# Kernel tuning notes

Hardware: AMD Instinct MI355X
Metric: run time of the kernel (lower is better)

## Reference

```python
import jax, jax.numpy as jnp
import numpy as np

N = 32768      # nodes
E = 524288     # edges (avg degree 16)
F = 64         # node_feat_dim
D = 64         # gnn_dim (= per-head out channels, concat=False)
ED = 32        # edge_feat_dim
L = 6          # num_layers
H = 2          # heads
C = D          # per-head channels
LN_EPS = 1e-5


def layer_norm(h, g, b):
    mu = jnp.mean(h, axis=-1, keepdims=True)
    var = jnp.mean((h - mu) ** 2, axis=-1, keepdims=True)
    return g * (h - mu) * jax.lax.rsqrt(var + LN_EPS) + b


def setup_inputs() -> dict:
    key = jax.random.key(0)
    ks = jax.random.split(key, 16)
    x = jax.random.normal(ks[0], (N, F), jnp.float32)
    edge_index = jax.random.randint(ks[1], (2, E), 0, N, jnp.int32)
    edge_attr = jax.random.normal(ks[2], (E, ED), jnp.float32)
    manual_gamma = 1.0 + 0.1 * jax.random.normal(ks[3], (L, D), jnp.float32)
    manual_beta = 0.1 * jax.random.normal(ks[4], (L, D), jnp.float32)
    # node_embed Linear(F, D)
    embed_W = jax.random.normal(ks[5], (F, D), jnp.float32) / np.float32(np.sqrt(F))
    embed_b = jnp.zeros((D,), jnp.float32)
    # per-layer LayerNorm affine params
    ln_gamma = jnp.ones((L, D), jnp.float32)
    ln_beta = jnp.zeros((L, D), jnp.float32)
    # per-layer GATConv params (shared lin for src/dst, PyG non-bipartite)
    lin_W = jax.random.normal(ks[6], (L, D, H * C), jnp.float32) / np.float32(np.sqrt(D))
    lin_edge_W = jax.random.normal(ks[7], (L, ED, H * C), jnp.float32) / np.float32(np.sqrt(ED))
    att_src = jax.random.normal(ks[8], (L, H, C), jnp.float32) / np.float32(np.sqrt(C))
    att_dst = jax.random.normal(ks[9], (L, H, C), jnp.float32) / np.float32(np.sqrt(C))
    att_edge = jax.random.normal(ks[10], (L, H, C), jnp.float32) / np.float32(np.sqrt(C))
    gat_bias = jnp.zeros((L, C), jnp.float32)
    # edge output head: Linear(2D+ED, D) -> ReLU -> Linear(D, 1)
    head_W1 = jax.random.normal(ks[11], (2 * D + ED, D), jnp.float32) / np.float32(np.sqrt(2 * D + ED))
    head_b1 = jnp.zeros((D,), jnp.float32)
    head_W2 = jax.random.normal(ks[12], (D, 1), jnp.float32) / np.float32(np.sqrt(D))
    head_b2 = jnp.zeros((1,), jnp.float32)
    return dict(x=x, edge_index=edge_index, edge_attr=edge_attr,
                manual_gamma=manual_gamma, manual_beta=manual_beta,
                embed_W=embed_W, embed_b=embed_b, ln_gamma=ln_gamma, ln_beta=ln_beta,
                lin_W=lin_W, lin_edge_W=lin_edge_W, att_src=att_src, att_dst=att_dst,
                att_edge=att_edge, gat_bias=gat_bias, head_W1=head_W1, head_b1=head_b1,
                head_W2=head_W2, head_b2=head_b2)


def reference(x, edge_index, edge_attr, manual_gamma, manual_beta,
              embed_W, embed_b, ln_gamma, ln_beta, lin_W, lin_edge_W,
              att_src, att_dst, att_edge, gat_bias, head_W1, head_b1,
              head_W2, head_b2):
    src, dst = edge_index[0], edge_index[1]
    # PyG GATConv default add_self_loops=True, fill_value='mean' for edge_attr
    loop = jnp.arange(N, dtype=edge_index.dtype)
    src_f = jnp.concatenate([src, loop])   # [E+N]
    dst_f = jnp.concatenate([dst, loop])
    deg = jax.ops.segment_sum(jnp.ones((E,), x.dtype), dst, num_segments=N)
    loop_attr = jax.ops.segment_sum(edge_attr, dst, num_segments=N) / jnp.maximum(deg, 1.0)[:, None]
    edge_attr_f = jnp.concatenate([edge_attr, loop_attr], axis=0)  # [E+N, ED]

    h = x @ embed_W + embed_b  # [N, D]
    for l in range(L):
        hn = layer_norm(h, ln_gamma[l], ln_beta[l])
        hm = manual_gamma[l][None, :] * hn + manual_beta[l][None, :]
        xh = (hm @ lin_W[l]).reshape(N, H, C)                      # [N,H,C]
        a_s = jnp.sum(xh * att_src[l][None], axis=-1)              # [N,H]
        a_d = jnp.sum(xh * att_dst[l][None], axis=-1)              # [N,H]
        eh = (edge_attr_f @ lin_edge_W[l]).reshape(-1, H, C)       # [E+N,H,C]
        a_e = jnp.sum(eh * att_edge[l][None], axis=-1)             # [E+N,H]
        alpha = jax.nn.leaky_relu(a_s[src_f] + a_d[dst_f] + a_e, 0.2)
        amax = jax.ops.segment_max(alpha, dst_f, num_segments=N)   # every node has a self-loop
        ex = jnp.exp(alpha - amax[dst_f])
        den = jax.ops.segment_sum(ex, dst_f, num_segments=N)
        w = ex / (den[dst_f] + 1e-16)                              # segment softmax [E+N,H]
        msg = xh[src_f] * w[..., None]                             # [E+N,H,C]
        out = jax.ops.segment_sum(msg, dst_f, num_segments=N)      # [N,H,C]
        h = jax.nn.relu(jnp.mean(out, axis=1) + gat_bias[l])       # concat=False -> head mean

    ef = jnp.concatenate([h[src], h[dst], edge_attr], axis=-1)     # [E, 2D+ED]
    hid = jax.nn.relu(ef @ head_W1 + head_b1)
    return (hid @ head_W2 + head_b2)[:, 0]                         # [E]
```

## Files before the change

### kernel.cpp

```cpp
#include <hip/hip_runtime.h>
#include <hip/hip_bf16.h>
#include <math.h>

#define NN 32768
#define EE 524288
#define LL 6

typedef __attribute__((ext_vector_type(8))) short short8;
typedef __attribute__((ext_vector_type(4))) float floatx4;

union U16x8 { short8 v; unsigned short u[8]; };

__device__ __forceinline__ unsigned short f2bf(float x) {
    union { float f; unsigned int u; } v; v.f = x;
    unsigned int r = v.u + 0x7fffu + ((v.u >> 16) & 1u);
    return (unsigned short)(r >> 16);
}
__device__ __forceinline__ float bf2f(unsigned short h) {
    union { unsigned int u; float f; } v; v.u = (unsigned int)h << 16;
    return v.f;
}


__global__ void deg_kernel(const int* __restrict__ dst, int* __restrict__ deg) {
    int e = blockIdx.x * 256 + threadIdx.x;
    if (e < EE) atomicAdd(&deg[dst[e]], 1);
}

__global__ __launch_bounds__(1024) void scan_kernel(const int* __restrict__ deg,
                                                    int* __restrict__ row_ptr) {
    __shared__ int bs[1024];
    int t = threadIdx.x;
    int base = t * 32;
    int loc[32];
    int s = 0;
#pragma unroll
    for (int i = 0; i < 32; ++i) { int v = deg[base + i]; loc[i] = s; s += v; }
    bs[t] = s;
    __syncthreads();
    for (int off = 1; off < 1024; off <<= 1) {
        int v = (t >= off) ? bs[t - off] : 0;
        __syncthreads();
        bs[t] += v;
        __syncthreads();
    }
    int pre = (t == 0) ? 0 : bs[t - 1];
#pragma unroll
    for (int i = 0; i < 32; ++i) row_ptr[base + i] = pre + loc[i];
    if (t == 1023) row_ptr[NN] = bs[1023];
}

__global__ void fill_kernel(const int* __restrict__ src, const int* __restrict__ dst,
                            const int* __restrict__ row_ptr, int* __restrict__ cnt,
                            int2* __restrict__ sedge) {
    int e = blockIdx.x * 256 + threadIdx.x;
    if (e >= EE) return;
    int d = dst[e];
    int pos = row_ptr[d] + atomicAdd(&cnt[d], 1);
    sedge[pos] = make_int2(src[e], e);
}

__global__ void vmake_kernel(const float* __restrict__ lin_edge_W,
                             const float* __restrict__ att_edge,
                             float* __restrict__ v) {
    int t = threadIdx.x;
    if (t >= 384) return;
    int l = t >> 6; int r = t & 63; int ed = r >> 1; int hh = r & 1;
    const float* w = lin_edge_W + l * 32 * 128 + ed * 128 + hh * 64;
    const float* a = att_edge + l * 128 + hh * 64;
    float s = 0.f;
#pragma unroll 8
    for (int c = 0; c < 64; ++c) s += w[c] * a[c];
    v[t] = s;
}

__global__ void vsmake_kernel(const float* __restrict__ lin_W,
                              const float* __restrict__ att_src,
                              const float* __restrict__ att_dst,
                              float* __restrict__ vs, float* __restrict__ vvd) {
    int l = blockIdx.x;
    int tid = threadIdx.x;
    int sel = tid >> 7, idx = tid & 127;
    int h = idx >> 6, k = idx & 63;
    const float* att = (sel ? att_dst : att_src) + l * 128 + h * 64;
    const float* wr = lin_W + ((size_t)l * 64 + k) * 128 + h * 64;
    float s = 0.f;
#pragma unroll 8
    for (int c = 0; c < 64; ++c) s += wr[c] * att[c];
    (sel ? vvd : vs)[l * 128 + idx] = s;
}

__global__ void ae_kernel(const float* __restrict__ edge_attr,
                          const float* __restrict__ v,
                          float* __restrict__ aeo) {
    __shared__ float sv[384];
    int tid = threadIdx.x;
    for (int i = tid; i < 384; i += 128) sv[i] = v[i];
    __syncthreads();
    int e = blockIdx.x * 128 + tid;
    if (e >= EE) return;
    float ea[32];
    const float4* p = (const float4*)(edge_attr + (size_t)e * 32);
#pragma unroll
    for (int i = 0; i < 8; ++i) {
        float4 f = p[i];
        ea[4 * i] = f.x; ea[4 * i + 1] = f.y; ea[4 * i + 2] = f.z; ea[4 * i + 3] = f.w;
    }
#pragma unroll
    for (int l = 0; l < LL; ++l) {
        float s0 = 0.f, s1 = 0.f;
#pragma unroll
        for (int ed = 0; ed < 32; ++ed) {
            float x = ea[ed];
            s0 += x * sv[l * 64 + ed * 2];
            s1 += x * sv[l * 64 + ed * 2 + 1];
        }
        aeo[((size_t)l * EE + e) * 2] = s0;
        aeo[((size_t)l * EE + e) * 2 + 1] = s1;
    }
}

__global__ __launch_bounds__(256) void embed_ln_kernel(
    const float* __restrict__ x, const float* __restrict__ W, const float* __restrict__ b,
    const float* __restrict__ ln_g, const float* __restrict__ ln_b,
    const float* __restrict__ mg, const float* __restrict__ mb,
    const float* __restrict__ vs0, const float* __restrict__ vd0,
    unsigned short* __restrict__ hm_bf, float* __restrict__ a_s, float* __restrict__ a_d) {
    __shared__ float xr[4][64];
    int w = threadIdx.x >> 6, j = threadIdx.x & 63;
    int n = blockIdx.x * 4 + w;
    xr[w][j] = x[(size_t)n * 64 + j];
    __syncthreads();
    float acc = b[j];
#pragma unroll 8
    for (int k = 0; k < 64; ++k) acc += xr[w][k] * W[k * 64 + j];
    float s = acc, sq = acc * acc;
    for (int off = 1; off < 64; off <<= 1) { s += __shfl_xor(s, off); sq += __shfl_xor(sq, off); }
    float mu = s * (1.f / 64.f);
    float var = sq * (1.f / 64.f) - mu * mu;
    float rs = rsqrtf(var + 1e-5f);
    float hm = mg[j] * (ln_g[j] * (acc - mu) * rs + ln_b[j]) + mb[j];
    hm_bf[(size_t)n * 64 + j] = f2bf(hm);
    float s0 = hm * vs0[j], s1 = hm * vs0[64 + j];
    float d0 = hm * vd0[j], d1 = hm * vd0[64 + j];
    for (int off = 1; off < 64; off <<= 1) {
        s0 += __shfl_xor(s0, off); s1 += __shfl_xor(s1, off);
        d0 += __shfl_xor(d0, off); d1 += __shfl_xor(d1, off);
    }
    if (j == 0) {
        a_s[n * 2] = s0; a_s[n * 2 + 1] = s1;
        a_d[n * 2] = d0; a_d[n * 2 + 1] = d1;
    }
}

__global__ __launch_bounds__(256) void wprep_kernel(const float* __restrict__ lin_W,
                                                    const float* __restrict__ head_W1,
                                                    unsigned short* __restrict__ gBhi,
                                                    unsigned short* __restrict__ gBlo) {
    int bb = blockIdx.x;
    int tid = threadIdx.x;
    unsigned short* dh = gBhi + (size_t)bb * 128 * 64;
    unsigned short* dl = gBlo + (size_t)bb * 128 * 64;
    if (bb < 6) {
        int n2 = tid & 63, kh = tid >> 6;
        U16x8 hh[4], ll[4];
        for (int kk = 0; kk < 32; ++kk) {
            int j = kh * 32 + kk;
            int h = j >> 6, k = j & 63;
            float wv = 0.5f * lin_W[((size_t)bb * 64 + k) * 128 + h * 64 + n2];
            unsigned short h16 = f2bf(wv);
            hh[kk >> 3].u[kk & 7] = h16;
            ll[kk >> 3].u[kk & 7] = f2bf(wv - bf2f(h16));
        }
#pragma unroll
        for (int c = 0; c < 4; ++c) {
            int cg = kh * 4 + c;
            int off = n2 * 128 + ((cg ^ (n2 & 15)) << 3);
            *(short8*)(dh + off) = hh[c].v;
            *(short8*)(dl + off) = ll[c].v;
        }
    } else {
        int n = tid & 127, kh = tid >> 7;
        U16x8 hh[4], ll[4];
        for (int kk = 0; kk < 32; ++kk) {
            int k = kh * 32 + kk;
            float wv = (n < 64) ? head_W1[k * 64 + n] : head_W1[(64 + k) * 64 + (n - 64)];
            unsigned short h16 = f2bf(wv);
            hh[kk >> 3].u[kk & 7] = h16;
            ll[kk >> 3].u[kk & 7] = f2bf(wv - bf2f(h16));
        }
#pragma unroll
        for (int c = 0; c < 4; ++c) {
            int cg = kh * 4 + c;
            int off = n * 64 + ((cg ^ (n & 7)) << 3);
            *(short8*)(dh + off) = hh[c].v;
            *(short8*)(dl + off) = ll[c].v;
        }
    }
}

__device__ __forceinline__ void fma8(uint4 pv, float w0, float w1, float* a0, float* a1) {
    unsigned int u[4] = {pv.x, pv.y, pv.z, pv.w};
#pragma unroll
    for (int j = 0; j < 4; ++j) {
        union { unsigned int q; float f; } lo, hi;
        lo.q = u[j] << 16; hi.q = u[j] & 0xffff0000u;
        a0[2 * j] += w0 * lo.f;  a1[2 * j] += w1 * lo.f;
        a0[2 * j + 1] += w0 * hi.f;  a1[2 * j + 1] += w1 * hi.f;
    }
}

__global__ __launch_bounds__(256) void aggregate5_kernel(
    const unsigned short* __restrict__ hm_bf, const float* __restrict__ a_s,
    const float* __restrict__ a_d, const float* __restrict__ aeo,
    const int* __restrict__ row_ptr, const int2* __restrict__ sedge,
    unsigned short* __restrict__ Abf) {
    __shared__ float2 swg[4][64];
    __shared__ int ssv[4][64];
    int w = threadIdx.x >> 6, lane = threadIdx.x & 63;
    int n = blockIdx.x * 4 + w;
    int slot = lane >> 3, ch = lane & 7;
    const float2* as2 = (const float2*)a_s;
    const float2* ae2 = (const float2*)aeo;
    const uint4* hmv = (const uint4*)hm_bf;
    float2 adn = ((const float2*)a_d)[n];
    float2 asn = as2[n];
    uint4 pvself = hmv[(size_t)n * 8 + ch];
    int beg = row_ptr[n], end = row_ptr[n + 1];

    float acc0[8] = {}, acc1[8] = {};
    float den0 = 0.f, den1 = 0.f, aex = 0.f, aey = 0.f;

    for (int cs = beg; cs < end; cs += 64) {
        int cnt = min(64, end - cs);
        float2 wpair = make_float2(0.f, 0.f);
        int sval = n;
        if (lane < cnt) {
            int2 se = sedge[cs + lane];
            float2 ae = ae2[se.y];
            float2 as = as2[se.x];
            aex += ae.x; aey += ae.y;
            float al0 = as.x + adn.x + ae.x; al0 = al0 > 0.f ? al0 : 0.2f * al0;
            float al1 = as.y + adn.y + ae.y; al1 = al1 > 0.f ? al1 : 0.2f * al1;
            wpair = make_float2(__expf(al0), __expf(al1));
            sval = se.x;
        }
        swg[w][lane] = wpair;
        ssv[w][lane] = sval;
        int ng2 = (cnt + 15) >> 4;
        for (int g2 = 0; g2 < ng2; ++g2) {
            int eA = g2 * 16 + slot, eB = g2 * 16 + 8 + slot;
            float2 wA = swg[w][eA];
            float2 wB = swg[w][eB];
            int svA = ssv[w][eA];
            int svB = ssv[w][eB];
            uint4 pvA = hmv[(size_t)svA * 8 + ch];
            uint4 pvB = hmv[(size_t)svB * 8 + ch];
            fma8(pvA, wA.x, wA.y, acc0, acc1);
            den0 += wA.x; den1 += wA.y;
            fma8(pvB, wB.x, wB.y, acc0, acc1);
            den0 += wB.x; den1 += wB.y;
        }
    }
#pragma unroll
    for (int m = 8; m < 64; m <<= 1) {
#pragma unroll
        for (int j = 0; j < 8; ++j) {
            acc0[j] += __shfl_xor(acc0[j], m);
            acc1[j] += __shfl_xor(acc1[j], m);
        }
        den0 += __shfl_xor(den0, m);
        den1 += __shfl_xor(den1, m);
        aex += __shfl_xor(aex, m);
        aey += __shfl_xor(aey, m);
    }
    if (slot == 0) {
        float invd = 1.f / fmaxf((float)(end - beg), 1.f);
        float al0 = asn.x + adn.x + aex * invd; al0 = al0 > 0.f ? al0 : 0.2f * al0;
        float al1 = asn.y + adn.y + aey * invd; al1 = al1 > 0.f ? al1 : 0.2f * al1;
        float ws0 = __expf(al0), ws1 = __expf(al1);
        fma8(pvself, ws0, ws1, acc0, acc1);
        den0 += ws0; den1 += ws1;
        float inv0 = 1.f / (den0 + 1e-16f), inv1 = 1.f / (den1 + 1e-16f);
        U16x8 h0, h1;
#pragma unroll
        for (int j = 0; j < 8; ++j) {
            h0.u[j] = f2bf(acc0[j] * inv0);
            h1.u[j] = f2bf(acc1[j] * inv1);
        }
        int i15 = n & 15;
        unsigned short* row = Abf + (size_t)n * 128;
        *(short8*)(row + ((ch ^ i15) << 3)) = h0.v;
        *(short8*)(row + (((8 + ch) ^ i15) << 3)) = h1.v;
    }
}

template <int LAST>
__global__ __launch_bounds__(256) void post_gemm(
    const unsigned short* __restrict__ Abf, const unsigned short* __restrict__ gBhi,
    const unsigned short* __restrict__ gBlo, const float* __restrict__ bias,
    const float* __restrict__ ln_g, const float* __restrict__ ln_b,
    const float* __restrict__ mg, const float* __restrict__ mb,
    const float* __restrict__ vsn, const float* __restrict__ vdn,
    unsigned short* __restrict__ hm_bf, float* __restrict__ a_s, float* __restrict__ a_d,
    float* __restrict__ hbuf) {
    __shared__ unsigned short Ahi[64 * 128];
    __shared__ unsigned short Bhi[64 * 128], Blo[64 * 128];
    int tid = threadIdx.x;
    {
        const uint4* sa = (const uint4*)(Abf + (size_t)blockIdx.x * 64 * 128);
        const uint4* sh = (const uint4*)gBhi;
        const uint4* sl = (const uint4*)gBlo;
        for (int i = tid; i < 1024; i += 256) {
            ((uint4*)Ahi)[i] = sa[i];
            ((uint4*)Bhi)[i] = sh[i];
            ((uint4*)Blo)[i] = sl[i];
        }
    }
    __syncthreads();

    int w = tid >> 6, lane = tid & 63, col = lane & 15, quad = lane >> 4;
    int m = w * 16 + col;
    floatx4 acc[4] = {};
#pragma unroll
    for (int s = 0; s < 4; ++s) {
        int ca = (quad + 4 * s) ^ col;
        short8 ahi = *(const short8*)(Ahi + m * 128 + ca * 8);
#pragma unroll
        for (int t = 0; t < 4; ++t) {
            int off = (t * 16 + col) * 128 + ca * 8;
            short8 bhi = *(const short8*)(Bhi + off);
            short8 blo = *(const short8*)(Blo + off);
            acc[t] = __builtin_amdgcn_mfma_f32_16x16x32_bf16(ahi, blo, acc[t], 0, 0, 0);
            acc[t] = __builtin_amdgcn_mfma_f32_16x16x32_bf16(ahi, bhi, acc[t], 0, 0, 0);
        }
    }
    int nodebase = blockIdx.x * 64 + w * 16;
    float bv[4];
#pragma unroll
    for (int t = 0; t < 4; ++t) bv[t] = bias[t * 16 + col];
    if (LAST) {
#pragma unroll
        for (int t = 0; t < 4; ++t)
#pragma unroll
            for (int r = 0; r < 4; ++r) {
                float hv = acc[t][r] + bv[t];
                hv = hv > 0.f ? hv : 0.f;
                hbuf[(size_t)(nodebase + quad * 4 + r) * 64 + t * 16 + col] = hv;
            }
    } else {
        float vsv[4], vsv1[4], vdv[4], vdv1[4], lg[4], lb[4], mgv[4], mbv[4];
#pragma unroll
        for (int t = 0; t < 4; ++t) {
            int c = t * 16 + col;
            vsv[t] = vsn[c]; vsv1[t] = vsn[64 + c];
            vdv[t] = vdn[c]; vdv1[t] = vdn[64 + c];
            lg[t] = ln_g[c]; lb[t] = ln_b[c];
            mgv[t] = mg[c]; mbv[t] = mb[c];
        }
#pragma unroll
        for (int r = 0; r < 4; ++r) {
            int node = nodebase + quad * 4 + r;
            float hv[4];
            float s = 0.f, sq = 0.f;
#pragma unroll
            for (int t = 0; t < 4; ++t) {
                float v = acc[t][r] + bv[t];
                v = v > 0.f ? v : 0.f;
                hv[t] = v;
                s += v; sq += v * v;
            }
            for (int off = 1; off < 16; off <<= 1) { s += __shfl_xor(s, off); sq += __shfl_xor(sq, off); }
            float mu = s * (1.f / 64.f);
            float var = sq * (1.f / 64.f) - mu * mu;
            float rs = rsqrtf(var + 1e-5f);
            float s0 = 0.f, s1 = 0.f, d0 = 0.f, d1 = 0.f;
#pragma unroll
            for (int t = 0; t < 4; ++t) {
                float hmv = mgv[t] * (lg[t] * (hv[t] - mu) * rs + lb[t]) + mbv[t];
                hm_bf[(size_t)node * 64 + t * 16 + col] = f2bf(hmv);
                s0 += hmv * vsv[t]; s1 += hmv * vsv1[t];
                d0 += hmv * vdv[t]; d1 += hmv * vdv1[t];
            }
            for (int off = 1; off < 16; off <<= 1) {
                s0 += __shfl_xor(s0, off); s1 += __shfl_xor(s1, off);
                d0 += __shfl_xor(d0, off); d1 += __shfl_xor(d1, off);
            }
            if (col == 0) {
                a_s[node * 2] = s0; a_s[node * 2 + 1] = s1;
                a_d[node * 2] = d0; a_d[node * 2 + 1] = d1;
            }
        }
    }
}

__global__ __launch_bounds__(256) void uv_gemm(
    const float* __restrict__ in, const unsigned short* __restrict__ gBhi,
    const unsigned short* __restrict__ gBlo, unsigned short* __restrict__ uv) {
    __shared__ unsigned short Ahi[64 * 64], Alo[64 * 64];
    __shared__ unsigned short Bhi[128 * 64], Blo[128 * 64];
    int tid = threadIdx.x;
    {
        const uint4* sh = (const uint4*)gBhi;
        const uint4* sl = (const uint4*)gBlo;
        for (int i = tid; i < 1024; i += 256) {
            ((uint4*)Bhi)[i] = sh[i];
            ((uint4*)Blo)[i] = sl[i];
        }
    }
    {
        int i = tid >> 2, q = tid & 3;
        int node = blockIdx.x * 64 + i;
        const float4* rp = (const float4*)(in + (size_t)node * 64);
        float4 va = rp[q * 4 + 0], vb = rp[q * 4 + 1], vc = rp[q * 4 + 2], vd = rp[q * 4 + 3];
        float f[16] = {va.x, va.y, va.z, va.w, vb.x, vb.y, vb.z, vb.w,
                       vc.x, vc.y, vc.z, vc.w, vd.x, vd.y, vd.z, vd.w};
        U16x8 hh[2], ll[2];
#pragma unroll
        for (int j = 0; j < 16; ++j) {
            unsigned short h16 = f2bf(f[j]);
            hh[j >> 3].u[j & 7] = h16;
            ll[j >> 3].u[j & 7] = f2bf(f[j] - bf2f(h16));
        }
#pragma unroll
        for (int c = 0; c < 2; ++c) {
            int cg = 2 * q + c;
            int off = i * 64 + ((cg ^ (i & 7)) << 3);
            *(short8*)(Ahi + off) = hh[c].v;
            *(short8*)(Alo + off) = ll[c].v;
        }
    }
    __syncthreads();
    int w = tid >> 6, lane = tid & 63, col = lane & 15, quad = lane >> 4;
    int m = w * 16 + col;
    floatx4 acc[8] = {};
#pragma unroll
    for (int s = 0; s < 2; ++s) {
        int ca = (quad + 4 * s) ^ (col & 7);
        short8 ahi = *(const short8*)(Ahi + m * 64 + ca * 8);
        short8 alo = *(const short8*)(Alo + m * 64 + ca * 8);
#pragma unroll
        for (int t = 0; t < 8; ++t) {
            int off = (t * 16 + col) * 64 + ca * 8;
            short8 bhi = *(const short8*)(Bhi + off);
            short8 blo = *(const short8*)(Blo + off);
            acc[t] = __builtin_amdgcn_mfma_f32_16x16x32_bf16(alo, bhi, acc[t], 0, 0, 0);
            acc[t] = __builtin_amdgcn_mfma_f32_16x16x32_bf16(ahi, blo, acc[t], 0, 0, 0);
            acc[t] = __builtin_amdgcn_mfma_f32_16x16x32_bf16(ahi, bhi, acc[t], 0, 0, 0);
        }
    }
    int nodebase = blockIdx.x * 64 + w * 16;
#pragma unroll
    for (int t = 0; t < 8; ++t)
#pragma unroll
        for (int r = 0; r < 4; ++r)
            uv[(size_t)(nodebase + quad * 4 + r) * 128 + t * 16 + col] = f2bf(acc[t][r]);
}


__global__ void w1c_split_kernel(const float* __restrict__ W1,
                                 unsigned short* __restrict__ w1chi,
                                 unsigned short* __restrict__ w1clo) {
    int tid = threadIdx.x;
    int n = tid & 63, kc = tid >> 6;
#pragma unroll
    for (int j = 0; j < 8; ++j) {
        int k = kc * 8 + j;
        float wv = W1[(128 + k) * 64 + n];
        unsigned short h16 = f2bf(wv);
        w1chi[n * 32 + k] = h16;
        w1clo[n * 32 + k] = f2bf(wv - bf2f(h16));
    }
}

__global__ __launch_bounds__(256) void head2_kernel(
    const unsigned short* __restrict__ uv, const int* __restrict__ src,
    const int* __restrict__ dst, const float* __restrict__ edge_attr,
    const unsigned short* __restrict__ w1chi, const unsigned short* __restrict__ w1clo,
    const float* __restrict__ b1, const float* __restrict__ W2,
    const float* __restrict__ b2, float* __restrict__ out) {
    __shared__ float g[64][68];
    __shared__ unsigned short Abf[64 * 40];
    __shared__ unsigned short Bh[64 * 40], Bl[64 * 40];
    __shared__ int sA[64], dA[64];
    int tid = threadIdx.x;
    int base = blockIdx.x * 64;
    if (tid < 64) sA[tid] = src[base + tid];
    else if (tid < 128) dA[tid - 64] = dst[base + tid - 64];
    {
        int n = tid >> 2, c = tid & 3;
        *(short8*)(Bh + n * 40 + c * 8) = *(const short8*)(w1chi + n * 32 + c * 8);
        *(short8*)(Bl + n * 40 + c * 8) = *(const short8*)(w1clo + n * 32 + c * 8);
    }
    {
        int e = tid >> 2, q = tid & 3;
        const float4* p = (const float4*)(edge_attr + (size_t)(base + e) * 32 + q * 8);
        float4 f0 = p[0], f1 = p[1];
        U16x8 u;
        u.u[0] = f2bf(f0.x); u.u[1] = f2bf(f0.y); u.u[2] = f2bf(f0.z); u.u[3] = f2bf(f0.w);
        u.u[4] = f2bf(f1.x); u.u[5] = f2bf(f1.y); u.u[6] = f2bf(f1.z); u.u[7] = f2bf(f1.w);
        *(short8*)(Abf + e * 40 + q * 8) = u.v;
    }
    __syncthreads();
    {
        int e = tid >> 2, q = tid & 3;
        const uint4* su = (const uint4*)(uv + (size_t)sA[e] * 128);
        const uint4* dv = (const uint4*)(uv + (size_t)dA[e] * 128);
        uint4 U0 = su[2 * q], U1 = su[2 * q + 1];
        uint4 V0 = dv[8 + 2 * q], V1 = dv[9 + 2 * q];
        const float4* b1p = (const float4*)(b1 + q * 16);
        float bb[16];
#pragma unroll
        for (int j = 0; j < 4; ++j) {
            float4 b4 = b1p[j];
            bb[4 * j] = b4.x; bb[4 * j + 1] = b4.y; bb[4 * j + 2] = b4.z; bb[4 * j + 3] = b4.w;
        }
        unsigned int uw[8] = {U0.x, U0.y, U0.z, U0.w, U1.x, U1.y, U1.z, U1.w};
        unsigned int vw[8] = {V0.x, V0.y, V0.z, V0.w, V1.x, V1.y, V1.z, V1.w};
        float* gr = &g[e][q * 16];
#pragma unroll
        for (int j = 0; j < 8; ++j) {
            gr[2 * j] = bf2f((unsigned short)(uw[j] & 0xffff)) +
                        bf2f((unsigned short)(vw[j] & 0xffff)) + bb[2 * j];
            gr[2 * j + 1] = bf2f((unsigned short)(uw[j] >> 16)) +
                            bf2f((unsigned short)(vw[j] >> 16)) + bb[2 * j + 1];
        }
    }
    __syncthreads();

    int lane = tid & 63, w = tid >> 6, col = lane & 15, quad = lane >> 4;
    short8 a = *(const short8*)(Abf + (w * 16 + col) * 40 + quad * 8);
    floatx4 acc[4] = {};
#pragma unroll
    for (int t = 0; t < 4; ++t) {
        int off = (t * 16 + col) * 40 + quad * 8;
        short8 bh = *(const short8*)(Bh + off);
        short8 bl = *(const short8*)(Bl + off);
        acc[t] = __builtin_amdgcn_mfma_f32_16x16x32_bf16(a, bl, acc[t], 0, 0, 0);
        acc[t] = __builtin_amdgcn_mfma_f32_16x16x32_bf16(a, bh, acc[t], 0, 0, 0);
    }
    float sv[4] = {0.f, 0.f, 0.f, 0.f};
#pragma unroll
    for (int t = 0; t < 4; ++t) {
        float w2v = W2[t * 16 + col];
#pragma unroll
        for (int r = 0; r < 4; ++r) {
            float hid = acc[t][r] + g[w * 16 + quad * 4 + r][t * 16 + col];
            hid = hid > 0.f ? hid : 0.f;
            sv[r] += hid * w2v;
        }
    }
    float b2v = b2[0];
#pragma unroll
    for (int r = 0; r < 4; ++r) {
        float v = sv[r];
        v += __shfl_xor(v, 1);
        v += __shfl_xor(v, 2);
        v += __shfl_xor(v, 4);
        v += __shfl_xor(v, 8);
        if (col == 0) out[base + w * 16 + quad * 4 + r] = v + b2v;
    }
}


extern "C" void kernel_launch(void* const* d_in, const int* in_sizes, int n_in,
                              void* d_out, int out_size, void* d_ws, size_t ws_size,
                              hipStream_t stream) {
    const float* x            = (const float*)d_in[0];
    const int*   edge_index   = (const int*)d_in[1];
    const float* edge_attr    = (const float*)d_in[2];
    const float* manual_gamma = (const float*)d_in[3];
    const float* manual_beta  = (const float*)d_in[4];
    const float* embed_W      = (const float*)d_in[5];
    const float* embed_b      = (const float*)d_in[6];
    const float* ln_gamma     = (const float*)d_in[7];
    const float* ln_beta      = (const float*)d_in[8];
    const float* lin_W        = (const float*)d_in[9];
    const float* lin_edge_W   = (const float*)d_in[10];
    const float* att_src      = (const float*)d_in[11];
    const float* att_dst      = (const float*)d_in[12];
    const float* att_edge     = (const float*)d_in[13];
    const float* gat_bias     = (const float*)d_in[14];
    const float* head_W1      = (const float*)d_in[15];
    const float* head_b1      = (const float*)d_in[16];
    const float* head_W2      = (const float*)d_in[17];
    const float* head_b2      = (const float*)d_in[18];
    float* out = (float*)d_out;

    const int* src = edge_index;
    const int* dst = edge_index + EE;

    char* ws = (char*)d_ws;
    size_t off = 0;
    auto alloc = [&](size_t bytes) {
        void* p = ws + off;
        off += (bytes + 255) & ~(size_t)255;
        return p;
    };
    int*   deg        = (int*)alloc(NN * 4);
    int*   row_ptr    = (int*)alloc((NN + 1) * 4);
    int*   cnt        = (int*)alloc(NN * 4);
    int2*  sedge      = (int2*)alloc((size_t)EE * 8);
    float* aeo        = (float*)alloc((size_t)LL * EE * 2 * 4);
    float* vbuf       = (float*)alloc(LL * 64 * 4);
    float* vs         = (float*)alloc(LL * 128 * 4);
    float* vvd        = (float*)alloc(LL * 128 * 4);
    float* hbuf       = (float*)alloc((size_t)NN * 64 * 4);
    float* a_s        = (float*)alloc((size_t)NN * 2 * 4);
    float* a_d        = (float*)alloc((size_t)NN * 2 * 4);
    unsigned short* Abf   = (unsigned short*)alloc((size_t)NN * 128 * 2);
    unsigned short* hm_bf = (unsigned short*)alloc((size_t)NN * 64 * 2);
    unsigned short* uvbuf = (unsigned short*)alloc((size_t)NN * 128 * 2);
    unsigned short* gBhi  = (unsigned short*)alloc((size_t)7 * 128 * 64 * 2);
    unsigned short* gBlo  = (unsigned short*)alloc((size_t)7 * 128 * 64 * 2);
    unsigned short* w1chi = (unsigned short*)alloc(64 * 32 * 2);
    unsigned short* w1clo = (unsigned short*)alloc(64 * 32 * 2);
    if (off > ws_size) return;

    hipMemsetAsync(deg, 0, NN * 4, stream);
    hipMemsetAsync(cnt, 0, NN * 4, stream);

    deg_kernel<<<EE / 256, 256, 0, stream>>>(dst, deg);
    scan_kernel<<<1, 1024, 0, stream>>>(deg, row_ptr);
    fill_kernel<<<EE / 256, 256, 0, stream>>>(src, dst, row_ptr, cnt, sedge);
    vmake_kernel<<<1, 384, 0, stream>>>(lin_edge_W, att_edge, vbuf);
    ae_kernel<<<EE / 128, 128, 0, stream>>>(edge_attr, vbuf, aeo);
    vsmake_kernel<<<LL, 256, 0, stream>>>(lin_W, att_src, att_dst, vs, vvd);
    wprep_kernel<<<7, 256, 0, stream>>>(lin_W, head_W1, gBhi, gBlo);
    w1c_split_kernel<<<1, 256, 0, stream>>>(head_W1, w1chi, w1clo);
    embed_ln_kernel<<<NN / 4, 256, 0, stream>>>(x, embed_W, embed_b, ln_gamma, ln_beta,
                                                manual_gamma, manual_beta, vs, vvd,
                                                hm_bf, a_s, a_d);

    for (int l = 0; l < LL; ++l) {
        aggregate5_kernel<<<NN / 4, 256, 0, stream>>>(
            hm_bf, a_s, a_d, aeo + (size_t)l * EE * 2, row_ptr, sedge, Abf);
        if (l < LL - 1) {
            post_gemm<0><<<NN / 64, 256, 0, stream>>>(
                Abf, gBhi + (size_t)l * 128 * 64, gBlo + (size_t)l * 128 * 64,
                gat_bias + l * 64, ln_gamma + (l + 1) * 64, ln_beta + (l + 1) * 64,
                manual_gamma + (l + 1) * 64, manual_beta + (l + 1) * 64,
                vs + (l + 1) * 128, vvd + (l + 1) * 128, hm_bf, a_s, a_d, nullptr);
        } else {
            post_gemm<1><<<NN / 64, 256, 0, stream>>>(
                Abf, gBhi + (size_t)l * 128 * 64, gBlo + (size_t)l * 128 * 64,
                gat_bias + l * 64, nullptr, nullptr, nullptr, nullptr,
                nullptr, nullptr, nullptr, nullptr, nullptr, hbuf);
        }
    }

    uv_gemm<<<NN / 64, 256, 0, stream>>>(hbuf, gBhi + (size_t)6 * 128 * 64,
                                         gBlo + (size_t)6 * 128 * 64, uvbuf);
    head2_kernel<<<EE / 64, 256, 0, stream>>>(uvbuf, src, dst, edge_attr, w1chi, w1clo,
                                              head_b1, head_W2, head_b2, out);
}
```

Measured before the change: 520.0 us.

## Fuse prep kernels, merge final post/uv GEMMs, shuffle-based aggregation, bf16 edge_attr

Merges the small weight-prep kernels into one launch and folds degree counting into the edge-attention kernel. The same kernel now also writes a bf16 copy of edge_attr, which the head reads instead of converting fp32 data itself. The last post GEMM and the uv GEMM become one kernel, so the fp32 hbuf round trip goes away. Aggregation passes weights and sources through wave shuffles rather than shared memory. This saves launches and memory traffic, at the cost of an extra bf16 edge_attr buffer and more work in the ae kernel.

```diff
diff --git a/kernel.cpp b/kernel.cpp
--- a/kernel.cpp
+++ b/kernel.cpp
@@ -22,13 +22,9 @@
 }
 
 
-__global__ void deg_kernel(const int* __restrict__ dst, int* __restrict__ deg) {
-    int e = blockIdx.x * 256 + threadIdx.x;
-    if (e < EE) atomicAdd(&deg[dst[e]], 1);
-}
-
 __global__ __launch_bounds__(1024) void scan_kernel(const int* __restrict__ deg,
-                                                    int* __restrict__ row_ptr) {
+                                                    int* __restrict__ row_ptr,
+                                                    int* __restrict__ cnt) {
     __shared__ int bs[1024];
     int t = threadIdx.x;
     int base = t * 32;
@@ -46,7 +42,7 @@
     }
     int pre = (t == 0) ? 0 : bs[t - 1];
 #pragma unroll
-    for (int i = 0; i < 32; ++i) row_ptr[base + i] = pre + loc[i];
+    for (int i = 0; i < 32; ++i) { row_ptr[base + i] = pre + loc[i]; cnt[base + i] = 0; }
     if (t == 1023) row_ptr[NN] = bs[1023];
 }
 
@@ -60,45 +56,99 @@
     sedge[pos] = make_int2(src[e], e);
 }
 
-__global__ void vmake_kernel(const float* __restrict__ lin_edge_W,
-                             const float* __restrict__ att_edge,
-                             float* __restrict__ v) {
-    int t = threadIdx.x;
-    if (t >= 384) return;
-    int l = t >> 6; int r = t & 63; int ed = r >> 1; int hh = r & 1;
-    const float* w = lin_edge_W + l * 32 * 128 + ed * 128 + hh * 64;
-    const float* a = att_edge + l * 128 + hh * 64;
-    float s = 0.f;
+__global__ __launch_bounds__(256) void smallprep_kernel(
+    const float* __restrict__ lin_W, const float* __restrict__ head_W1,
+    const float* __restrict__ lin_edge_W, const float* __restrict__ att_edge,
+    const float* __restrict__ att_src, const float* __restrict__ att_dst,
+    unsigned short* __restrict__ gBhi, unsigned short* __restrict__ gBlo,
+    float* __restrict__ vbuf, float* __restrict__ vs, float* __restrict__ vvd,
+    unsigned short* __restrict__ w1chi, unsigned short* __restrict__ w1clo) {
+    int bb = blockIdx.x;
+    int tid = threadIdx.x;
+    if (bb < 7) {
+        unsigned short* dh = gBhi + (size_t)bb * 128 * 64;
+        unsigned short* dl = gBlo + (size_t)bb * 128 * 64;
+        if (bb < 6) {
+            int n2 = tid & 63, kh = tid >> 6;
+            U16x8 hh[4], ll[4];
+            for (int kk = 0; kk < 32; ++kk) {
+                int j = kh * 32 + kk;
+                int h = j >> 6, k = j & 63;
+                float wv = 0.5f * lin_W[((size_t)bb * 64 + k) * 128 + h * 64 + n2];
+                unsigned short h16 = f2bf(wv);
+                hh[kk >> 3].u[kk & 7] = h16;
+                ll[kk >> 3].u[kk & 7] = f2bf(wv - bf2f(h16));
+            }
+#pragma unroll
+            for (int c = 0; c < 4; ++c) {
+                int cg = kh * 4 + c;
+                int off = n2 * 128 + ((cg ^ (n2 & 15)) << 3);
+                *(short8*)(dh + off) = hh[c].v;
+                *(short8*)(dl + off) = ll[c].v;
+            }
+        } else {
+            int n = tid & 127, kh = tid >> 7;
+            U16x8 hh[4], ll[4];
+            for (int kk = 0; kk < 32; ++kk) {
+                int k = kh * 32 + kk;
+                float wv = (n < 64) ? head_W1[k * 64 + n] : head_W1[(64 + k) * 64 + (n - 64)];
+                unsigned short h16 = f2bf(wv);
+                hh[kk >> 3].u[kk & 7] = h16;
+                ll[kk >> 3].u[kk & 7] = f2bf(wv - bf2f(h16));
+            }
+#pragma unroll
+            for (int c = 0; c < 4; ++c) {
+                int cg = kh * 4 + c;
+                int off = n * 64 + ((cg ^ (n & 7)) << 3);
+                *(short8*)(dh + off) = hh[c].v;
+                *(short8*)(dl + off) = ll[c].v;
+            }
+        }
+    } else if (bb == 7) {
+        for (int t = tid; t < 384; t += 256) {
+            int l = t / 64; int r = t & 63; int ed = r >> 1; int hh = r & 1;
+            const float* w = lin_edge_W + l * 32 * 128 + ed * 128 + hh * 64;
+            const float* a = att_edge + l * 128 + hh * 64;
+            float s = 0.f;
 #pragma unroll 8
-    for (int c = 0; c < 64; ++c) s += w[c] * a[c];
-    v[t] = s;
-}
-
-__global__ void vsmake_kernel(const float* __restrict__ lin_W,
-                              const float* __restrict__ att_src,
-                              const float* __restrict__ att_dst,
-                              float* __restrict__ vs, float* __restrict__ vvd) {
-    int l = blockIdx.x;
-    int tid = threadIdx.x;
-    int sel = tid >> 7, idx = tid & 127;
-    int h = idx >> 6, k = idx & 63;
-    const float* att = (sel ? att_dst : att_src) + l * 128 + h * 64;
-    const float* wr = lin_W + ((size_t)l * 64 + k) * 128 + h * 64;
-    float s = 0.f;
+            for (int c = 0; c < 64; ++c) s += w[c] * a[c];
+            vbuf[t] = s;
+        }
+        int n = tid & 63, kc = tid >> 6;
+#pragma unroll
+        for (int j = 0; j < 8; ++j) {
+            int k = kc * 8 + j;
+            float wv = head_W1[(128 + k) * 64 + n];
+            unsigned short h16 = f2bf(wv);
+            w1chi[n * 32 + k] = h16;
+            w1clo[n * 32 + k] = f2bf(wv - bf2f(h16));
+        }
+    } else {
+        int l = bb - 8;
+        int sel = tid >> 7, idx = tid & 127;
+        int h = idx >> 6, k = idx & 63;
+        const float* att = (sel ? att_dst : att_src) + l * 128 + h * 64;
+        const float* wr = lin_W + ((size_t)l * 64 + k) * 128 + h * 64;
+        float s = 0.f;
 #pragma unroll 8
-    for (int c = 0; c < 64; ++c) s += wr[c] * att[c];
-    (sel ? vvd : vs)[l * 128 + idx] = s;
-}
-
-__global__ void ae_kernel(const float* __restrict__ edge_attr,
-                          const float* __restrict__ v,
-                          float* __restrict__ aeo) {
+        for (int c = 0; c < 64; ++c) s += wr[c] * att[c];
+        (sel ? vvd : vs)[l * 128 + idx] = s;
+    }
+}
+
+__global__ void ae_deg_kernel(const float* __restrict__ edge_attr,
+                              const int* __restrict__ dst,
+                              const float* __restrict__ v,
+                              float* __restrict__ aeo,
+                              unsigned short* __restrict__ eabf,
+                              int* __restrict__ deg) {
     __shared__ float sv[384];
     int tid = threadIdx.x;
     for (int i = tid; i < 384; i += 128) sv[i] = v[i];
     __syncthreads();
     int e = blockIdx.x * 128 + tid;
     if (e >= EE) return;
+    atomicAdd(&deg[dst[e]], 1);
     float ea[32];
     const float4* p = (const float4*)(edge_attr + (size_t)e * 32);
 #pragma unroll
@@ -106,6 +156,11 @@
         float4 f = p[i];
         ea[4 * i] = f.x; ea[4 * i + 1] = f.y; ea[4 * i + 2] = f.z; ea[4 * i + 3] = f.w;
     }
+    U16x8 ub[4];
+#pragma unroll
+    for (int j = 0; j < 32; ++j) ub[j >> 3].u[j & 7] = f2bf(ea[j]);
+#pragma unroll
+    for (int j = 0; j < 4; ++j) *(short8*)(eabf + (size_t)e * 32 + j * 8) = ub[j].v;
 #pragma unroll
     for (int l = 0; l < LL; ++l) {
         float s0 = 0.f, s1 = 0.f;
@@ -153,52 +208,6 @@
     }
 }
 
-__global__ __launch_bounds__(256) void wprep_kernel(const float* __restrict__ lin_W,
-                                                    const float* __restrict__ head_W1,
-                                                    unsigned short* __restrict__ gBhi,
-                                                    unsigned short* __restrict__ gBlo) {
-    int bb = blockIdx.x;
-    int tid = threadIdx.x;
-    unsigned short* dh = gBhi + (size_t)bb * 128 * 64;
-    unsigned short* dl = gBlo + (size_t)bb * 128 * 64;
-    if (bb < 6) {
-        int n2 = tid & 63, kh = tid >> 6;
-        U16x8 hh[4], ll[4];
-        for (int kk = 0; kk < 32; ++kk) {
-            int j = kh * 32 + kk;
-            int h = j >> 6, k = j & 63;
-            float wv = 0.5f * lin_W[((size_t)bb * 64 + k) * 128 + h * 64 + n2];
-            unsigned short h16 = f2bf(wv);
-            hh[kk >> 3].u[kk & 7] = h16;
-            ll[kk >> 3].u[kk & 7] = f2bf(wv - bf2f(h16));
-        }
-#pragma unroll
-        for (int c = 0; c < 4; ++c) {
-            int cg = kh * 4 + c;
-            int off = n2 * 128 + ((cg ^ (n2 & 15)) << 3);
-            *(short8*)(dh + off) = hh[c].v;
-            *(short8*)(dl + off) = ll[c].v;
-        }
-    } else {
-        int n = tid & 127, kh = tid >> 7;
-        U16x8 hh[4], ll[4];
-        for (int kk = 0; kk < 32; ++kk) {
-            int k = kh * 32 + kk;
-            float wv = (n < 64) ? head_W1[k * 64 + n] : head_W1[(64 + k) * 64 + (n - 64)];
-            unsigned short h16 = f2bf(wv);
-            hh[kk >> 3].u[kk & 7] = h16;
-            ll[kk >> 3].u[kk & 7] = f2bf(wv - bf2f(h16));
-        }
-#pragma unroll
-        for (int c = 0; c < 4; ++c) {
-            int cg = kh * 4 + c;
-            int off = n * 64 + ((cg ^ (n & 7)) << 3);
-            *(short8*)(dh + off) = hh[c].v;
-            *(short8*)(dl + off) = ll[c].v;
-        }
-    }
-}
-
 __device__ __forceinline__ void fma8(uint4 pv, float w0, float w1, float* a0, float* a1) {
     unsigned int u[4] = {pv.x, pv.y, pv.z, pv.w};
 #pragma unroll
@@ -210,13 +219,11 @@
     }
 }
 
-__global__ __launch_bounds__(256) void aggregate5_kernel(
+__global__ __launch_bounds__(256) void aggregate6_kernel(
     const unsigned short* __restrict__ hm_bf, const float* __restrict__ a_s,
     const float* __restrict__ a_d, const float* __restrict__ aeo,
     const int* __restrict__ row_ptr, const int2* __restrict__ sedge,
     unsigned short* __restrict__ Abf) {
-    __shared__ float2 swg[4][64];
-    __shared__ int ssv[4][64];
     int w = threadIdx.x >> 6, lane = threadIdx.x & 63;
     int n = blockIdx.x * 4 + w;
     int slot = lane >> 3, ch = lane & 7;
@@ -233,7 +240,7 @@
 
     for (int cs = beg; cs < end; cs += 64) {
         int cnt = min(64, end - cs);
-        float2 wpair = make_float2(0.f, 0.f);
+        float w0v = 0.f, w1v = 0.f;
         int sval = n;
         if (lane < cnt) {
             int2 se = sedge[cs + lane];
@@ -242,25 +249,27 @@
             aex += ae.x; aey += ae.y;
             float al0 = as.x + adn.x + ae.x; al0 = al0 > 0.f ? al0 : 0.2f * al0;
             float al1 = as.y + adn.y + ae.y; al1 = al1 > 0.f ? al1 : 0.2f * al1;
-            wpair = make_float2(__expf(al0), __expf(al1));
+            w0v = __expf(al0);
+            w1v = __expf(al1);
             sval = se.x;
         }
-        swg[w][lane] = wpair;
-        ssv[w][lane] = sval;
         int ng2 = (cnt + 15) >> 4;
         for (int g2 = 0; g2 < ng2; ++g2) {
-            int eA = g2 * 16 + slot, eB = g2 * 16 + 8 + slot;
-            float2 wA = swg[w][eA];
-            float2 wB = swg[w][eB];
-            int svA = ssv[w][eA];
-            int svB = ssv[w][eB];
+            int eA = g2 * 16 + slot, eB = eA + 8;
+            int svA = __shfl(sval, eA), svB = __shfl(sval, eB);
+            float wA0 = __shfl(w0v, eA), wA1 = __shfl(w1v, eA);
+            float wB0 = __shfl(w0v, eB), wB1 = __shfl(w1v, eB);
             uint4 pvA = hmv[(size_t)svA * 8 + ch];
             uint4 pvB = hmv[(size_t)svB * 8 + ch];
-            fma8(pvA, wA.x, wA.y, acc0, acc1);
-            den0 += wA.x; den1 += wA.y;
-            fma8(pvB, wB.x, wB.y, acc0, acc1);
-            den0 += wB.x; den1 += wB.y;
-        }
+            fma8(pvA, wA0, wA1, acc0, acc1);
+            den0 += wA0; den1 += wA1;
+            fma8(pvB, wB0, wB1, acc0, acc1);
+            den0 += wB0; den1 += wB1;
+        }
+    }
+    for (int m = 1; m < 8; m <<= 1) {
+        aex += __shfl_xor(aex, m);
+        aey += __shfl_xor(aey, m);
     }
 #pragma unroll
     for (int m = 8; m < 64; m <<= 1) {
@@ -295,15 +304,13 @@
     }
 }
 
-template <int LAST>
 __global__ __launch_bounds__(256) void post_gemm(
     const unsigned short* __restrict__ Abf, const unsigned short* __restrict__ gBhi,
     const unsigned short* __restrict__ gBlo, const float* __restrict__ bias,
     const float* __restrict__ ln_g, const float* __restrict__ ln_b,
     const float* __restrict__ mg, const float* __restrict__ mb,
     const float* __restrict__ vsn, const float* __restrict__ vdn,
-    unsigned short* __restrict__ hm_bf, float* __restrict__ a_s, float* __restrict__ a_d,
-    float* __restrict__ hbuf) {
+    unsigned short* __restrict__ hm_bf, float* __restrict__ a_s, float* __restrict__ a_d) {
     __shared__ unsigned short Ahi[64 * 128];
     __shared__ unsigned short Bhi[64 * 128], Blo[64 * 128];
     int tid = threadIdx.x;
@@ -339,114 +346,131 @@
     float bv[4];
 #pragma unroll
     for (int t = 0; t < 4; ++t) bv[t] = bias[t * 16 + col];
-    if (LAST) {
-#pragma unroll
-        for (int t = 0; t < 4; ++t)
-#pragma unroll
-            for (int r = 0; r < 4; ++r) {
-                float hv = acc[t][r] + bv[t];
-                hv = hv > 0.f ? hv : 0.f;
-                hbuf[(size_t)(nodebase + quad * 4 + r) * 64 + t * 16 + col] = hv;
-            }
-    } else {
-        float vsv[4], vsv1[4], vdv[4], vdv1[4], lg[4], lb[4], mgv[4], mbv[4];
+    float vsv[4], vsv1[4], vdv[4], vdv1[4], lg[4], lb[4], mgv[4], mbv[4];
+#pragma unroll
+    for (int t = 0; t < 4; ++t) {
+        int c = t * 16 + col;
+        vsv[t] = vsn[c]; vsv1[t] = vsn[64 + c];
+        vdv[t] = vdn[c]; vdv1[t] = vdn[64 + c];
+        lg[t] = ln_g[c]; lb[t] = ln_b[c];
+        mgv[t] = mg[c]; mbv[t] = mb[c];
+    }
+#pragma unroll
+    for (int r = 0; r < 4; ++r) {
+        int node = nodebase + quad * 4 + r;
+        float hv[4];
+        float s = 0.f, sq = 0.f;
 #pragma unroll
         for (int t = 0; t < 4; ++t) {
-            int c = t * 16 + col;
-            vsv[t] = vsn[c]; vsv1[t] = vsn[64 + c];
-            vdv[t] = vdn[c]; vdv1[t] = vdn[64 + c];
-            lg[t] = ln_g[c]; lb[t] = ln_b[c];
-            mgv[t] = mg[c]; mbv[t] = mb[c];
-        }
-#pragma unroll
-        for (int r = 0; r < 4; ++r) {
-            int node = nodebase + quad * 4 + r;
-            float hv[4];
-            float s = 0.f, sq = 0.f;
-#pragma unroll
-            for (int t = 0; t < 4; ++t) {
-                float v = acc[t][r] + bv[t];
-                v = v > 0.f ? v : 0.f;
-                hv[t] = v;
-                s += v; sq += v * v;
-            }
-            for (int off = 1; off < 16; off <<= 1) { s += __shfl_xor(s, off); sq += __shfl_xor(sq, off); }
-            float mu = s * (1.f / 64.f);
-            float var = sq * (1.f / 64.f) - mu * mu;
-            float rs = rsqrtf(var + 1e-5f);
-            float s0 = 0.f, s1 = 0.f, d0 = 0.f, d1 = 0.f;
-#pragma unroll
-            for (int t = 0; t < 4; ++t) {
-                float hmv = mgv[t] * (lg[t] * (hv[t] - mu) * rs + lb[t]) + mbv[t];
-                hm_bf[(size_t)node * 64 + t * 16 + col] = f2bf(hmv);
-                s0 += hmv * vsv[t]; s1 += hmv * vsv1[t];
-                d0 += hmv * vdv[t]; d1 += hmv * vdv1[t];
-            }
-            for (int off = 1; off < 16; off <<= 1) {
-                s0 += __shfl_xor(s0, off); s1 += __shfl_xor(s1, off);
-                d0 += __shfl_xor(d0, off); d1 += __shfl_xor(d1, off);
-            }
-            if (col == 0) {
-                a_s[node * 2] = s0; a_s[node * 2 + 1] = s1;
-                a_d[node * 2] = d0; a_d[node * 2 + 1] = d1;
-            }
-        }
-    }
-}
-
-__global__ __launch_bounds__(256) void uv_gemm(
-    const float* __restrict__ in, const unsigned short* __restrict__ gBhi,
-    const unsigned short* __restrict__ gBlo, unsigned short* __restrict__ uv) {
-    __shared__ unsigned short Ahi[64 * 64], Alo[64 * 64];
-    __shared__ unsigned short Bhi[128 * 64], Blo[128 * 64];
+            float v = acc[t][r] + bv[t];
+            v = v > 0.f ? v : 0.f;
+            hv[t] = v;
+            s += v; sq += v * v;
+        }
+        for (int off = 1; off < 16; off <<= 1) { s += __shfl_xor(s, off); sq += __shfl_xor(sq, off); }
+        float mu = s * (1.f / 64.f);
+        float var = sq * (1.f / 64.f) - mu * mu;
+        float rs = rsqrtf(var + 1e-5f);
+        float s0 = 0.f, s1 = 0.f, d0 = 0.f, d1 = 0.f;
+#pragma unroll
+        for (int t = 0; t < 4; ++t) {
+            float hmv = mgv[t] * (lg[t] * (hv[t] - mu) * rs + lb[t]) + mbv[t];
+            hm_bf[(size_t)node * 64 + t * 16 + col] = f2bf(hmv);
+            s0 += hmv * vsv[t]; s1 += hmv * vsv1[t];
+            d0 += hmv * vdv[t]; d1 += hmv * vdv1[t];
+        }
+        for (int off = 1; off < 16; off <<= 1) {
+            s0 += __shfl_xor(s0, off); s1 += __shfl_xor(s1, off);
+            d0 += __shfl_xor(d0, off); d1 += __shfl_xor(d1, off);
+        }
+        if (col == 0) {
+            a_s[node * 2] = s0; a_s[node * 2 + 1] = s1;
+            a_d[node * 2] = d0; a_d[node * 2 + 1] = d1;
+        }
+    }
+}
+
+__global__ __launch_bounds__(256) void postuv_gemm(
+    const unsigned short* __restrict__ Abf, const unsigned short* __restrict__ gB5hi,
+    const unsigned short* __restrict__ gB5lo, const float* __restrict__ bias,
+    const unsigned short* __restrict__ gB6hi, const unsigned short* __restrict__ gB6lo,
+    unsigned short* __restrict__ uv) {
+    __shared__ unsigned short lds[24576];
+    unsigned short* Ahi  = lds;
+    unsigned short* B5hi = lds + 8192;
+    unsigned short* B5lo = lds + 16384;
+    unsigned short* A2hi = lds;
+    unsigned short* A2lo = lds + 4096;
+    unsigned short* B6hi = lds + 8192;
+    unsigned short* B6lo = lds + 16384;
     int tid = threadIdx.x;
     {
-        const uint4* sh = (const uint4*)gBhi;
-        const uint4* sl = (const uint4*)gBlo;
+        const uint4* sa = (const uint4*)(Abf + (size_t)blockIdx.x * 64 * 128);
+        const uint4* sh = (const uint4*)gB5hi;
+        const uint4* sl = (const uint4*)gB5lo;
         for (int i = tid; i < 1024; i += 256) {
-            ((uint4*)Bhi)[i] = sh[i];
-            ((uint4*)Blo)[i] = sl[i];
-        }
-    }
-    {
-        int i = tid >> 2, q = tid & 3;
-        int node = blockIdx.x * 64 + i;
-        const float4* rp = (const float4*)(in + (size_t)node * 64);
-        float4 va = rp[q * 4 + 0], vb = rp[q * 4 + 1], vc = rp[q * 4 + 2], vd = rp[q * 4 + 3];
-        float f[16] = {va.x, va.y, va.z, va.w, vb.x, vb.y, vb.z, vb.w,
-                       vc.x, vc.y, vc.z, vc.w, vd.x, vd.y, vd.z, vd.w};
-        U16x8 hh[2], ll[2];
-#pragma unroll
-        for (int j = 0; j < 16; ++j) {
-            unsigned short h16 = f2bf(f[j]);
-            hh[j >> 3].u[j & 7] = h16;
-            ll[j >> 3].u[j & 7] = f2bf(f[j] - bf2f(h16));
-        }
-#pragma unroll
-        for (int c = 0; c < 2; ++c) {
-            int cg = 2 * q + c;
-            int off = i * 64 + ((cg ^ (i & 7)) << 3);
-            *(short8*)(Ahi + off) = hh[c].v;
-            *(short8*)(Alo + off) = ll[c].v;
-        }
-    }
-    __syncthreads();
+            ((uint4*)Ahi)[i] = sa[i];
+            ((uint4*)B5hi)[i] = sh[i];
+            ((uint4*)B5lo)[i] = sl[i];
+        }
+    }
+    __syncthreads();
+
     int w = tid >> 6, lane = tid & 63, col = lane & 15, quad = lane >> 4;
     int m = w * 16 + col;
-    floatx4 acc[8] = {};
+    floatx4 acc[4] = {};
+#pragma unroll
+    for (int s = 0; s < 4; ++s) {
+        int ca = (quad + 4 * s) ^ col;
+        short8 ahi = *(const short8*)(Ahi + m * 128 + ca * 8);
+#pragma unroll
+        for (int t = 0; t < 4; ++t) {
+            int off = (t * 16 + col) * 128 + ca * 8;
+            short8 bhi = *(const short8*)(B5hi + off);
+            short8 blo = *(const short8*)(B5lo + off);
+            acc[t] = __builtin_amdgcn_mfma_f32_16x16x32_bf16(ahi, blo, acc[t], 0, 0, 0);
+            acc[t] = __builtin_amdgcn_mfma_f32_16x16x32_bf16(ahi, bhi, acc[t], 0, 0, 0);
+        }
+    }
+    float bv[4];
+#pragma unroll
+    for (int t = 0; t < 4; ++t) bv[t] = bias[t * 16 + col];
+    __syncthreads();
+#pragma unroll
+    for (int t = 0; t < 4; ++t) {
+        int c = t * 16 + col;
+        int cg = c >> 3, cr = c & 7;
+#pragma unroll
+        for (int r = 0; r < 4; ++r) {
+            float v = acc[t][r] + bv[t];
+            v = v > 0.f ? v : 0.f;
+            int i = w * 16 + quad * 4 + r;
+            int off = i * 64 + ((cg ^ (i & 7)) << 3) + cr;
+            unsigned short hh = f2bf(v);
+            A2hi[off] = hh;
+            A2lo[off] = f2bf(v - bf2f(hh));
+        }
+    }
+    for (int i = tid; i < 1024; i += 256) {
+        ((uint4*)B6hi)[i] = ((const uint4*)gB6hi)[i];
+        ((uint4*)B6lo)[i] = ((const uint4*)gB6lo)[i];
+    }
+    __syncthreads();
+
+    floatx4 acc2[8] = {};
 #pragma unroll
     for (int s = 0; s < 2; ++s) {
         int ca = (quad + 4 * s) ^ (col & 7);
-        short8 ahi = *(const short8*)(Ahi + m * 64 + ca * 8);
-        short8 alo = *(const short8*)(Alo + m * 64 + ca * 8);
+        short8 a2h = *(const short8*)(A2hi + m * 64 + ca * 8);
+        short8 a2l = *(const short8*)(A2lo + m * 64 + ca * 8);
 #pragma unroll
         for (int t = 0; t < 8; ++t) {
             int off = (t * 16 + col) * 64 + ca * 8;
-            short8 bhi = *(const short8*)(Bhi + off);
-            short8 blo = *(const short8*)(Blo + off);
-            acc[t] = __builtin_amdgcn_mfma_f32_16x16x32_bf16(alo, bhi, acc[t], 0, 0, 0);
-            acc[t] = __builtin_amdgcn_mfma_f32_16x16x32_bf16(ahi, blo, acc[t], 0, 0, 0);
-            acc[t] = __builtin_amdgcn_mfma_f32_16x16x32_bf16(ahi, bhi, acc[t], 0, 0, 0);
+            short8 bh = *(const short8*)(B6hi + off);
+            short8 bl = *(const short8*)(B6lo + off);
+            acc2[t] = __builtin_amdgcn_mfma_f32_16x16x32_bf16(a2l, bh, acc2[t], 0, 0, 0);
+            acc2[t] = __builtin_amdgcn_mfma_f32_16x16x32_bf16(a2h, bl, acc2[t], 0, 0, 0);
+            acc2[t] = __builtin_amdgcn_mfma_f32_16x16x32_bf16(a2h, bh, acc2[t], 0, 0, 0);
         }
     }
     int nodebase = blockIdx.x * 64 + w * 16;
@@ -454,28 +478,12 @@
     for (int t = 0; t < 8; ++t)
 #pragma unroll
         for (int r = 0; r < 4; ++r)
-            uv[(size_t)(nodebase + quad * 4 + r) * 128 + t * 16 + col] = f2bf(acc[t][r]);
-}
-
-
-__global__ void w1c_split_kernel(const float* __restrict__ W1,
-                                 unsigned short* __restrict__ w1chi,
-                                 unsigned short* __restrict__ w1clo) {
-    int tid = threadIdx.x;
-    int n = tid & 63, kc = tid >> 6;
-#pragma unroll
-    for (int j = 0; j < 8; ++j) {
-        int k = kc * 8 + j;
-        float wv = W1[(128 + k) * 64 + n];
-        unsigned short h16 = f2bf(wv);
-        w1chi[n * 32 + k] = h16;
-        w1clo[n * 32 + k] = f2bf(wv - bf2f(h16));
-    }
+            uv[(size_t)(nodebase + quad * 4 + r) * 128 + t * 16 + col] = f2bf(acc2[t][r]);
 }
 
 __global__ __launch_bounds__(256) void head2_kernel(
     const unsigned short* __restrict__ uv, const int* __restrict__ src,
-    const int* __restrict__ dst, const float* __restrict__ edge_attr,
+    const int* __restrict__ dst, const unsigned short* __restrict__ eabf,
     const unsigned short* __restrict__ w1chi, const unsigned short* __restrict__ w1clo,
     const float* __restrict__ b1, const float* __restrict__ W2,
     const float* __restrict__ b2, float* __restrict__ out) {
@@ -494,12 +502,7 @@
     }
     {
         int e = tid >> 2, q = tid & 3;
-        const float4* p = (const float4*)(edge_attr + (size_t)(base + e) * 32 + q * 8);
-        float4 f0 = p[0], f1 = p[1];
-        U16x8 u;
-        u.u[0] = f2bf(f0.x); u.u[1] = f2bf(f0.y); u.u[2] = f2bf(f0.z); u.u[3] = f2bf(f0.w);
-        u.u[4] = f2bf(f1.x); u.u[5] = f2bf(f1.y); u.u[6] = f2bf(f1.z); u.u[7] = f2bf(f1.w);
-        *(short8*)(Abf + e * 40 + q * 8) = u.v;
+        *(short8*)(Abf + e * 40 + q * 8) = *(const short8*)(eabf + (size_t)(base + e) * 32 + q * 8);
     }
     __syncthreads();
     {
@@ -605,12 +608,12 @@
     float* vbuf       = (float*)alloc(LL * 64 * 4);
     float* vs         = (float*)alloc(LL * 128 * 4);
     float* vvd        = (float*)alloc(LL * 128 * 4);
-    float* hbuf       = (float*)alloc((size_t)NN * 64 * 4);
     float* a_s        = (float*)alloc((size_t)NN * 2 * 4);
     float* a_d        = (float*)alloc((size_t)NN * 2 * 4);
     unsigned short* Abf   = (unsigned short*)alloc((size_t)NN * 128 * 2);
     unsigned short* hm_bf = (unsigned short*)alloc((size_t)NN * 64 * 2);
     unsigned short* uvbuf = (unsigned short*)alloc((size_t)NN * 128 * 2);
+    unsigned short* eabf  = (unsigned short*)alloc((size_t)EE * 32 * 2);
     unsigned short* gBhi  = (unsigned short*)alloc((size_t)7 * 128 * 64 * 2);
     unsigned short* gBlo  = (unsigned short*)alloc((size_t)7 * 128 * 64 * 2);
     unsigned short* w1chi = (unsigned short*)alloc(64 * 32 * 2);
@@ -618,39 +621,34 @@
     if (off > ws_size) return;
 
     hipMemsetAsync(deg, 0, NN * 4, stream);
-    hipMemsetAsync(cnt, 0, NN * 4, stream);
-
-    deg_kernel<<<EE / 256, 256, 0, stream>>>(dst, deg);
-    scan_kernel<<<1, 1024, 0, stream>>>(deg, row_ptr);
+
+    smallprep_kernel<<<14, 256, 0, stream>>>(lin_W, head_W1, lin_edge_W, att_edge,
+                                             att_src, att_dst, gBhi, gBlo, vbuf,
+                                             vs, vvd, w1chi, w1clo);
+    ae_deg_kernel<<<EE / 128, 128, 0, stream>>>(edge_attr, dst, vbuf, aeo, eabf, deg);
+    scan_kernel<<<1, 1024, 0, stream>>>(deg, row_ptr, cnt);
     fill_kernel<<<EE / 256, 256, 0, stream>>>(src, dst, row_ptr, cnt, sedge);
-    vmake_kernel<<<1, 384, 0, stream>>>(lin_edge_W, att_edge, vbuf);
-    ae_kernel<<<EE / 128, 128, 0, stream>>>(edge_attr, vbuf, aeo);
-    vsmake_kernel<<<LL, 256, 0, stream>>>(lin_W, att_src, att_dst, vs, vvd);
-    wprep_kernel<<<7, 256, 0, stream>>>(lin_W, head_W1, gBhi, gBlo);
-    w1c_split_kernel<<<1, 256, 0, stream>>>(head_W1, w1chi, w1clo);
     embed_ln_kernel<<<NN / 4, 256, 0, stream>>>(x, embed_W, embed_b, ln_gamma, ln_beta,
                                                 manual_gamma, manual_beta, vs, vvd,
                                                 hm_bf, a_s, a_d);
 
     for (int l = 0; l < LL; ++l) {
-        aggregate5_kernel<<<NN / 4, 256, 0, stream>>>(
+        aggregate6_kernel<<<NN / 4, 256, 0, stream>>>(
             hm_bf, a_s, a_d, aeo + (size_t)l * EE * 2, row_ptr, sedge, Abf);
         if (l < LL - 1) {
-            post_gemm<0><<<NN / 64, 256, 0, stream>>>(
+            post_gemm<<<NN / 64, 256, 0, stream>>>(
                 Abf, gBhi + (size_t)l * 128 * 64, gBlo + (size_t)l * 128 * 64,
                 gat_bias + l * 64, ln_gamma + (l + 1) * 64, ln_beta + (l + 1) * 64,
                 manual_gamma + (l + 1) * 64, manual_beta + (l + 1) * 64,
-                vs + (l + 1) * 128, vvd + (l + 1) * 128, hm_bf, a_s, a_d, nullptr);
+                vs + (l + 1) * 128, vvd + (l + 1) * 128, hm_bf, a_s, a_d);
         } else {
-            post_gemm<1><<<NN / 64, 256, 0, stream>>>(
+            postuv_gemm<<<NN / 64, 256, 0, stream>>>(
                 Abf, gBhi + (size_t)l * 128 * 64, gBlo + (size_t)l * 128 * 64,
-                gat_bias + l * 64, nullptr, nullptr, nullptr, nullptr,
-                nullptr, nullptr, nullptr, nullptr, nullptr, hbuf);
-        }
-    }
-
-    uv_gemm<<<NN / 64, 256, 0, stream>>>(hbuf, gBhi + (size_t)6 * 128 * 64,
-                                         gBlo + (size_t)6 * 128 * 64, uvbuf);
-    head2_kernel<<<EE / 64, 256, 0, stream>>>(uvbuf, src, dst, edge_attr, w1chi, w1clo,
+                gat_bias + l * 64, gBhi + (size_t)6 * 128 * 64,
+                gBlo + (size_t)6 * 128 * 64, uvbuf);
+        }
+    }
+
+    head2_kernel<<<EE / 64, 256, 0, stream>>>(uvbuf, src, dst, eabf, w1chi, w1clo,
                                               head_b1, head_W2, head_b2, out);
 }
```

Result: no change. 512.0 us (-1.5%).
